# Optimization experiments

Hardware: AMD Instinct MI355X
Metric: run time of the kernel (lower is better)

The kernel has to match this reference:

```python
import jax, jax.numpy as jnp
import numpy as np

N_NODES = 100000
N_EDGES = 1600000
IN_DIM = 128
HIDDEN = 128
OUT_DIM = 10
N_GRAPHS = 512
N_LAYERS = 3


def setup_inputs() -> dict:
    key = jax.random.key(0)
    ks = jax.random.split(key, 12)
    s_in = 1.0 / np.sqrt(IN_DIM)
    s_h = 1.0 / np.sqrt(HIDDEN)
    return {
        "x": jax.random.normal(ks[0], (N_NODES, IN_DIM), jnp.float32),
        "lin1_w": jax.random.normal(ks[1], (IN_DIM, HIDDEN), jnp.float32) * s_in,
        "lin1_b": jnp.zeros((HIDDEN,), jnp.float32),
        "gcn_w": jax.random.normal(ks[2], (N_LAYERS, HIDDEN, HIDDEN), jnp.float32) * s_h,
        "gcn_b": jnp.zeros((N_LAYERS, HIDDEN), jnp.float32),
        "lin_out_w": jax.random.normal(ks[3], (HIDDEN, HIDDEN), jnp.float32) * s_h,
        "lin_out_b": jnp.zeros((HIDDEN,), jnp.float32),
        "cls_w": jax.random.normal(ks[4], (HIDDEN, OUT_DIM), jnp.float32) * s_h,
        "cls_b": jnp.zeros((OUT_DIM,), jnp.float32),
        "edge_index": jax.random.randint(ks[5], (2, N_EDGES), 0, N_NODES, jnp.int64),
        "batch": jnp.sort(jax.random.randint(ks[6], (N_NODES,), 0, N_GRAPHS, jnp.int64)),
    }


def reference(x, lin1_w, lin1_b, gcn_w, gcn_b, lin_out_w, lin_out_b, cls_w, cls_b, edge_index, batch):
    n = x.shape[0]
    # GCNConv normalization with added self-loops (PyG default)
    row, col = edge_index[0], edge_index[1]
    loop = jnp.arange(n)
    row2 = jnp.concatenate([row, loop])  # source (message origin)
    col2 = jnp.concatenate([col, loop])  # target (aggregation index)
    deg = jax.ops.segment_sum(jnp.ones_like(col2, dtype=x.dtype), col2, num_segments=n)
    dinv = jax.lax.rsqrt(jnp.maximum(deg, 1.0))
    norm = (dinv[row2] * dinv[col2])[:, None]  # [E+N, 1]

    counts = jax.ops.segment_sum(jnp.ones((n,), x.dtype), batch, num_segments=N_GRAPHS)
    counts = jnp.maximum(counts, 1.0)[:, None]

    def readout_mean(h):  # global_mean_pool -> [G, H]
        return jax.ops.segment_sum(h, batch, num_segments=N_GRAPHS) / counts

    # lin1 + elu (dropout = identity in eval mode)
    h = jax.nn.elu(x @ lin1_w + lin1_b)
    reps = readout_mean(h)  # readout_layers[0]; l_sum accumulates layer reps
    for i in range(N_LAYERS):
        hw = h @ gcn_w[i]                       # [N, H]
        msg = norm * hw[row2]                   # gather + scale
        agg = jax.ops.segment_sum(msg, col2, num_segments=n)  # scatter-add
        h = jax.nn.elu(agg + gcn_b[i])          # GCNConv bias then NaOp act
        # pooling op is 'none' (remove_pooling=True): graph unchanged
        reps = reps + readout_mean(h)           # readout_layers[i+1], summed by LaOp 'l_sum'
    g = jax.nn.elu(reps @ lin_out_w + lin_out_b)
    logits = g @ cls_w + cls_b
    return jax.nn.log_softmax(logits, axis=-1)
```

## Files before the change

### kernel.cpp

```cpp
#include <hip/hip_runtime.h>
#include <hip/hip_bf16.h>
#include <math.h>

#define NN 100000
#define NE 1600000
#define HID 128
#define NG 512
#define NB 512
#define RB 196

typedef unsigned short ushort_t;
typedef __attribute__((ext_vector_type(8))) short bf16x8;
typedef __attribute__((ext_vector_type(8))) unsigned short ushort8_t;
typedef __attribute__((ext_vector_type(4))) float f32x4;

__device__ __forceinline__ ushort_t f2bf(float v) {
    unsigned u = __float_as_uint(v);
    unsigned r = (u + 0x7FFF + ((u >> 16) & 1)) >> 16;
    return (ushort_t)r;
}
__device__ __forceinline__ float bf2f(ushort_t u) {
    return __uint_as_float((unsigned)u << 16);
}

__global__ __launch_bounds__(256) void hist_and_prepw(const int* __restrict__ ecol, int* __restrict__ ghist, int E,
                                                      const float* __restrict__ lin1_w,
                                                      const float* __restrict__ gcn_w,
                                                      ushort_t* __restrict__ wt_hi,
                                                      ushort_t* __restrict__ wt_lo) {
    if (blockIdx.x < 512) {
        __shared__ int lh[NB];
        for (int i = threadIdx.x; i < NB; i += 256) lh[i] = 0;
        __syncthreads();
        for (int e = blockIdx.x * 256 + threadIdx.x; e < E; e += 512 * 256)
            atomicAdd(&lh[ecol[e] / RB], 1);
        __syncthreads();
        for (int i = threadIdx.x; i < NB; i += 256) {
            int c = lh[i];
            if (c) atomicAdd(&ghist[i], c);
        }
    } else {
        int mb = blockIdx.x - 512;
        int m = mb >> 3;
        int chunk = mb & 7;
        const float* W = (m == 0) ? lin1_w : gcn_w + (size_t)(m - 1) * 16384;
        ushort_t* hi = wt_hi + (size_t)m * 16384;
        ushort_t* lo = wt_lo + (size_t)m * 16384;
        for (int i = chunk * 2048 + threadIdx.x; i < (chunk + 1) * 2048; i += 256) {
            int j = i & 7;
            int lane = (i >> 3) & 63;
            int ks = (i >> 9) & 3;
            int ct = (i >> 11) & 7;
            int n = ct * 16 + (lane & 15);
            int k = ks * 32 + (lane >> 4) * 8 + j;
            float v = W[k * 128 + n];
            ushort_t h = f2bf(v);
            hi[i] = h;
            lo[i] = f2bf(v - bf2f(h));
        }
    }
}

__global__ __launch_bounds__(NB) void bucket_scan(const int* __restrict__ ghist, int* __restrict__ brp,
                                                  int* __restrict__ gcur, int* __restrict__ rp,
                                                  const int* __restrict__ batch, float* __restrict__ invcnt) {
    __shared__ int s[NB];
    int t = threadIdx.x;
    int v = ghist[t];
    s[t] = v;
    __syncthreads();
    for (int off = 1; off < NB; off <<= 1) {
        int x = (t >= off) ? s[t - off] : 0;
        __syncthreads();
        s[t] += x;
        __syncthreads();
    }
    int ex = s[t] - v;
    brp[t] = ex;
    gcur[t] = ex;
    if (t == NB - 1) { brp[NB] = s[t]; rp[NN] = s[t]; }

    int lo = 0, hi = NN;
    while (lo < hi) { int m = (lo + hi) >> 1; if (batch[m] < t) lo = m + 1; else hi = m; }
    int s0 = lo;
    lo = 0; hi = NN;
    while (lo < hi) { int m = (lo + hi) >> 1; if (batch[m] < t + 1) lo = m + 1; else hi = m; }
    int c = lo - s0;
    invcnt[t] = 1.0f / (float)(c > 0 ? c : 1);
}

#define CHUNK 4096
__global__ __launch_bounds__(256) void partition_edges(const int* __restrict__ erow, const int* __restrict__ ecol,
                                                       int* __restrict__ gcur, unsigned int* __restrict__ pairs, int E) {
    __shared__ int cnt[NB];
    __shared__ int base[NB];
    const int t = threadIdx.x;
    const int e0 = blockIdx.x * CHUNK;
    const int e1 = min(e0 + CHUNK, E);
    for (int i = t; i < NB; i += 256) cnt[i] = 0;
    __syncthreads();
    for (int e = e0 + t; e < e1; e += 256) atomicAdd(&cnt[ecol[e] / RB], 1);
    __syncthreads();
    for (int i = t; i < NB; i += 256) {
        int c = cnt[i];
        base[i] = c ? atomicAdd(&gcur[i], c) : 0;
        cnt[i] = 0;
    }
    __syncthreads();
    for (int e = e0 + t; e < e1; e += 256) {
        int d = ecol[e];
        int b = d / RB;
        int off = atomicAdd(&cnt[b], 1);
        pairs[base[b] + off] = ((unsigned)erow[e] << 8) | (unsigned)(d - b * RB);
    }
}

__global__ __launch_bounds__(256) void bucket_fill(const unsigned int* __restrict__ pairs, const int* __restrict__ brp,
                                                   int* __restrict__ rp, float* __restrict__ dinv,
                                                   int* __restrict__ csrc) {
    __shared__ int cnt[RB];
    __shared__ int cur[RB];
    __shared__ int sc[256];
    const int b = blockIdx.x, t = threadIdx.x;
    const int nbase = b * RB;
    const int s = brp[b], e = brp[b + 1];
    for (int i = t; i < RB; i += 256) cnt[i] = 0;
    __syncthreads();
    for (int i = s + t; i < e; i += 256) atomicAdd(&cnt[pairs[i] & 255u], 1);
    __syncthreads();
    int v = (t < RB) ? cnt[t] : 0;
    sc[t] = v;
    __syncthreads();
    for (int off = 1; off < 256; off <<= 1) {
        int x = (t >= off) ? sc[t - off] : 0;
        __syncthreads();
        sc[t] += x;
        __syncthreads();
    }
    if (t < RB) {
        int ex = s + sc[t] - v;
        int node = nbase + t;
        if (node < NN) {
            rp[node] = ex;
            dinv[node] = rsqrtf((float)v + 1.0f);
        }
        cur[t] = ex;
    }
    __syncthreads();
    for (int i = s + t; i < e; i += 256) {
        unsigned int p = pairs[i];
        int slot = atomicAdd(&cur[p & 255u], 1);
        csrc[slot] = (int)(p >> 8);
    }
}

template<bool F32A, int MODE>
__global__ __launch_bounds__(256) void gemm_mfma(const float* __restrict__ A,
                                                 const ushort_t* __restrict__ a_bf,
                                                 const ushort_t* __restrict__ wt_hi,
                                                 const ushort_t* __restrict__ wt_lo,
                                                 const float* __restrict__ bias,
                                                 const float* __restrict__ dinv,
                                                 ushort_t* __restrict__ out0,
                                                 int N) {
    const int lane = threadIdx.x & 63;
    const int wid = threadIdx.x >> 6;
    const int rowBase = blockIdx.x * 128 + wid * 32;
    const int l15 = lane & 15, lg = lane >> 4;

    f32x4 acc[2][8];
#pragma unroll
    for (int rt = 0; rt < 2; ++rt)
#pragma unroll
        for (int ct = 0; ct < 8; ++ct) acc[rt][ct] = (f32x4){0.f, 0.f, 0.f, 0.f};

#pragma unroll
    for (int ks = 0; ks < 4; ++ks) {
        bf16x8 ahi[2], alo[2];
#pragma unroll
        for (int rt = 0; rt < 2; ++rt) {
            int r = rowBase + rt * 16 + l15;
            if (F32A) {
                float av[8];
                if (r < N) {
                    const float* ap = A + (size_t)r * 128 + ks * 32 + lg * 8;
                    float4 a0 = *(const float4*)(ap);
                    float4 a1 = *(const float4*)(ap + 4);
                    av[0] = a0.x; av[1] = a0.y; av[2] = a0.z; av[3] = a0.w;
                    av[4] = a1.x; av[5] = a1.y; av[6] = a1.z; av[7] = a1.w;
                } else {
#pragma unroll
                    for (int j = 0; j < 8; ++j) av[j] = 0.f;
                }
#pragma unroll
                for (int j = 0; j < 8; ++j) {
                    ushort_t h = f2bf(av[j]);
                    ahi[rt][j] = (short)h;
                    alo[rt][j] = (short)f2bf(av[j] - bf2f(h));
                }
            } else {
                if (r < N) {
                    ahi[rt] = *(const bf16x8*)(a_bf + (size_t)r * 128 + ks * 32 + lg * 8);
                } else {
                    bf16x8 z = {0, 0, 0, 0, 0, 0, 0, 0};
                    ahi[rt] = z;
                }
            }
        }
#pragma unroll
        for (int ct = 0; ct < 8; ++ct) {
            size_t boff = (size_t)(((ct * 4 + ks) * 64 + lane) * 8);
            bf16x8 bhi = *(const bf16x8*)(wt_hi + boff);
            bf16x8 blo = *(const bf16x8*)(wt_lo + boff);
            acc[0][ct] = __builtin_amdgcn_mfma_f32_16x16x32_bf16(ahi[0], bhi, acc[0][ct], 0, 0, 0);
            acc[1][ct] = __builtin_amdgcn_mfma_f32_16x16x32_bf16(ahi[1], bhi, acc[1][ct], 0, 0, 0);
            acc[0][ct] = __builtin_amdgcn_mfma_f32_16x16x32_bf16(ahi[0], blo, acc[0][ct], 0, 0, 0);
            acc[1][ct] = __builtin_amdgcn_mfma_f32_16x16x32_bf16(ahi[1], blo, acc[1][ct], 0, 0, 0);
            if (F32A) {
                acc[0][ct] = __builtin_amdgcn_mfma_f32_16x16x32_bf16(alo[0], bhi, acc[0][ct], 0, 0, 0);
                acc[1][ct] = __builtin_amdgcn_mfma_f32_16x16x32_bf16(alo[1], bhi, acc[1][ct], 0, 0, 0);
            }
        }
    }

#pragma unroll
    for (int rt = 0; rt < 2; ++rt) {
#pragma unroll
        for (int reg = 0; reg < 4; ++reg) {
            int row = rowBase + rt * 16 + lg * 4 + reg;
            if (row >= N) continue;
            if (MODE == 0) {
#pragma unroll
                for (int ct = 0; ct < 8; ++ct) {
                    int colc = ct * 16 + l15;
                    float v = acc[rt][ct][reg] + bias[colc];
                    v = v > 0.f ? v : expf(v) - 1.f;
                    out0[(size_t)row * 128 + colc] = f2bf(v);
                }
            } else {
                float dv = dinv[row];
#pragma unroll
                for (int ct = 0; ct < 8; ++ct) {
                    int colc = ct * 16 + l15;
                    out0[(size_t)row * 128 + colc] = f2bf(acc[rt][ct][reg] * dv);
                }
            }
        }
    }
}

__global__ __launch_bounds__(256) void gather_agg(const int* __restrict__ rp,
                                                  const int* __restrict__ csrc,
                                                  const float* __restrict__ dinv,
                                                  const ushort_t* __restrict__ hwb,
                                                  const float* __restrict__ bias,
                                                  const int* __restrict__ batch,
                                                  const float* __restrict__ invcnt,
                                                  float* __restrict__ reps,
                                                  ushort_t* __restrict__ h_out) {
    __shared__ float sh[16][128];
    __shared__ int gid[16];
    const int v0 = blockIdx.x * 16;
    const int ns = (int)(threadIdx.x >> 4);
    int v = v0 + ns;
    int c8 = (int)(threadIdx.x & 15) << 3;
    if (threadIdx.x < 16) {
        int bidx = v0 + (int)threadIdx.x;
        if (bidx > NN - 1) bidx = NN - 1;
        gid[threadIdx.x] = batch[bidx];
    }

    float acc[8] = {};
    if (v < NN) {
        int s = rp[v], e = rp[v + 1];
        int i = s;
        for (; i + 16 <= e; i += 16) {
            int u[16];
#pragma unroll
            for (int k = 0; k < 16; ++k) u[k] = csrc[i + k];
            ushort8_t r[16];
#pragma unroll
            for (int k = 0; k < 16; ++k) r[k] = *(const ushort8_t*)(hwb + (size_t)u[k] * 128 + c8);
#pragma unroll
            for (int k = 0; k < 16; ++k)
#pragma unroll
                for (int j = 0; j < 8; ++j) acc[j] += bf2f(r[k][j]);
        }
        for (; i + 8 <= e; i += 8) {
            int u[8];
#pragma unroll
            for (int k = 0; k < 8; ++k) u[k] = csrc[i + k];
            ushort8_t r[8];
#pragma unroll
            for (int k = 0; k < 8; ++k) r[k] = *(const ushort8_t*)(hwb + (size_t)u[k] * 128 + c8);
#pragma unroll
            for (int k = 0; k < 8; ++k)
#pragma unroll
                for (int j = 0; j < 8; ++j) acc[j] += bf2f(r[k][j]);
        }
        for (; i < e; ++i) {
            int u = csrc[i];
            ushort8_t r0 = *(const ushort8_t*)(hwb + (size_t)u * 128 + c8);
#pragma unroll
            for (int j = 0; j < 8; ++j) acc[j] += bf2f(r0[j]);
        }

        float di = dinv[v];
        ushort8_t sv = *(const ushort8_t*)(hwb + (size_t)v * 128 + c8);
        ushort8_t o;
#pragma unroll
        for (int j = 0; j < 8; ++j) {
            float t = di * (acc[j] + bf2f(sv[j])) + bias[c8 + j];
            t = t > 0.f ? t : expf(t) - 1.f;
            acc[j] = t;
            o[j] = f2bf(t);
        }
        *(ushort8_t*)(h_out + (size_t)v * 128 + c8) = o;
    } else {
#pragma unroll
        for (int j = 0; j < 8; ++j) acc[j] = 0.f;
    }

#pragma unroll
    for (int j = 0; j < 8; ++j) sh[ns][c8 + j] = acc[j];
    __syncthreads();
    if (threadIdx.x < 128) {
        int c = (int)threadIdx.x;
        int nvalid = NN - v0;
        if (nvalid > 16) nvalid = 16;
        float run = sh[0][c];
        int cg = gid[0];
        for (int k = 1; k < nvalid; ++k) {
            int g2 = gid[k];
            if (g2 != cg) {
                unsafeAtomicAdd(&reps[(size_t)cg * 128 + c], run * invcnt[cg]);
                run = 0.f;
                cg = g2;
            }
            run += sh[k][c];
        }
        unsafeAtomicAdd(&reps[(size_t)cg * 128 + c], run * invcnt[cg]);
    }
}

__global__ __launch_bounds__(256) void readout(const ushort_t* __restrict__ h,
                                               const int* __restrict__ batch,
                                               int n, float* __restrict__ reps) {
    int g = blockIdx.x >> 2;
    int part = blockIdx.x & 3;
    int lo = 0, hi = n;
    while (lo < hi) { int m = (lo + hi) >> 1; if (batch[m] < g) lo = m + 1; else hi = m; }
    int s = lo;
    lo = 0; hi = n;
    while (lo < hi) { int m = (lo + hi) >> 1; if (batch[m] < g + 1) lo = m + 1; else hi = m; }
    int e = lo;

    __shared__ float sh[16][128];
    int ns = (int)(threadIdx.x >> 4);
    int L  = (int)(threadIdx.x & 15);
    int c8 = L << 3;
    float acc[8] = {};
    for (int v = s + part + ns * 4; v < e; v += 64) {
        ushort8_t t = *(const ushort8_t*)(h + (size_t)v * 128 + c8);
#pragma unroll
        for (int j = 0; j < 8; ++j) acc[j] += bf2f(t[j]);
    }
#pragma unroll
    for (int j = 0; j < 8; ++j) sh[ns][c8 + j] = acc[j];
    __syncthreads();
    if (threadIdx.x < 128) {
        int c = (int)threadIdx.x;
        float sum = 0.f;
#pragma unroll
        for (int k = 0; k < 16; ++k) sum += sh[k][c];
        float cnt = (float)(e - s > 0 ? e - s : 1);
        unsafeAtomicAdd(&reps[(size_t)g * 128 + c], sum / cnt);
    }
}

__global__ __launch_bounds__(256) void gemm128(const float* __restrict__ A,
                                               const float* __restrict__ W,
                                               const float* __restrict__ bias,
                                               float* __restrict__ out,
                                               int N, int applyElu) {
    __shared__ float xs[64][128];
    __shared__ float ws[128][64];
    const int tid = threadIdx.x;
    const int rowBase = blockIdx.x * 64;
    const int colBase = blockIdx.y * 64;
#pragma unroll
    for (int it = 0; it < 8; ++it) {
        int idx = it * 256 + tid;
        int r = idx >> 5;
        int c4 = (idx & 31) << 2;
        int gr = rowBase + r;
        float4 v = make_float4(0.f, 0.f, 0.f, 0.f);
        if (gr < N) v = *(const float4*)(A + (size_t)gr * 128 + c4);
        *(float4*)(&xs[r][c4]) = v;
    }
#pragma unroll
    for (int it = 0; it < 8; ++it) {
        int idx = it * 256 + tid;
        int k = idx >> 4;
        int c4 = (idx & 15) << 2;
        *(float4*)(&ws[k][c4]) = *(const float4*)(W + (size_t)k * 128 + colBase + c4);
    }
    __syncthreads();
    const int rowg = tid >> 4, colg = tid & 15;
    const int r0 = rowg * 4, c0 = colg * 4;
    float acc[4][4] = {};
#pragma unroll 2
    for (int kb = 0; kb < 128; kb += 4) {
        float4 xr[4], wr[4];
#pragma unroll
        for (int i = 0; i < 4; ++i) xr[i] = *(const float4*)(&xs[r0 + i][kb]);
#pragma unroll
        for (int kk = 0; kk < 4; ++kk) wr[kk] = *(const float4*)(&ws[kb + kk][c0]);
#pragma unroll
        for (int i = 0; i < 4; ++i) {
            const float* xp = (const float*)&xr[i];
#pragma unroll
            for (int kk = 0; kk < 4; ++kk) {
                float xv = xp[kk];
                acc[i][0] = fmaf(xv, wr[kk].x, acc[i][0]);
                acc[i][1] = fmaf(xv, wr[kk].y, acc[i][1]);
                acc[i][2] = fmaf(xv, wr[kk].z, acc[i][2]);
                acc[i][3] = fmaf(xv, wr[kk].w, acc[i][3]);
            }
        }
    }
    float4 b4 = make_float4(0.f, 0.f, 0.f, 0.f);
    if (bias) b4 = *(const float4*)(bias + colBase + c0);
#pragma unroll
    for (int i = 0; i < 4; ++i) {
        int gr = rowBase + r0 + i;
        if (gr < N) {
            float4 o;
            o.x = acc[i][0] + b4.x;
            o.y = acc[i][1] + b4.y;
            o.z = acc[i][2] + b4.z;
            o.w = acc[i][3] + b4.w;
            if (applyElu) {
                o.x = o.x > 0.f ? o.x : expf(o.x) - 1.f;
                o.y = o.y > 0.f ? o.y : expf(o.y) - 1.f;
                o.z = o.z > 0.f ? o.z : expf(o.z) - 1.f;
                o.w = o.w > 0.f ? o.w : expf(o.w) - 1.f;
            }
            *(float4*)(out + (size_t)gr * 128 + colBase + c0) = o;
        }
    }
}

__global__ __launch_bounds__(64) void cls_logsoftmax(const float* __restrict__ g,
                                                     const float* __restrict__ cw,
                                                     const float* __restrict__ cb,
                                                     float* __restrict__ out) {
    int r = blockIdx.x;
    __shared__ float row[128];
    __shared__ float lg[10];
    int t = threadIdx.x;
    row[t] = g[(size_t)r * 128 + t];
    row[64 + t] = g[(size_t)r * 128 + 64 + t];
    __syncthreads();
    if (t < 10) {
        float a = cb[t];
        for (int k = 0; k < 128; ++k) a = fmaf(row[k], cw[k * 10 + t], a);
        lg[t] = a;
    }
    __syncthreads();
    if (t == 0) {
        float m = lg[0];
#pragma unroll
        for (int j = 1; j < 10; ++j) m = fmaxf(m, lg[j]);
        float se = 0.f;
#pragma unroll
        for (int j = 0; j < 10; ++j) se += expf(lg[j] - m);
        float L = logf(se);
#pragma unroll
        for (int j = 0; j < 10; ++j) out[(size_t)r * 10 + j] = lg[j] - m - L;
    }
}

extern "C" void kernel_launch(void* const* d_in, const int* in_sizes, int n_in,
                              void* d_out, int out_size, void* d_ws, size_t ws_size,
                              hipStream_t stream) {
    const float* x        = (const float*)d_in[0];
    const float* lin1_w   = (const float*)d_in[1];
    const float* lin1_b   = (const float*)d_in[2];
    const float* gcn_w    = (const float*)d_in[3];
    const float* gcn_b    = (const float*)d_in[4];
    const float* lin_out_w= (const float*)d_in[5];
    const float* lin_out_b= (const float*)d_in[6];
    const float* cls_w    = (const float*)d_in[7];
    const float* cls_b    = (const float*)d_in[8];
    const int*   ei       = (const int*)d_in[9];
    const int*   batch    = (const int*)d_in[10];
    float* out = (float*)d_out;

    const int* erow = ei;
    const int* ecol = ei + NE;

    ushort_t* h     = (ushort_t*)d_ws;
    ushort_t* hwb   = h + (size_t)NN * 128;
    float*    dinv  = (float*)(hwb + (size_t)NN * 128);
    float*    reps  = dinv + NN;
    float*    gbuf  = reps + (size_t)NG * 128;
    float*    invcnt= gbuf + (size_t)NG * 128;
    int*      rp    = (int*)(invcnt + NG);
    int*      csrc  = rp + NN + 1;
    int*      ghist = csrc + NE;
    int*      brp   = ghist + NB;
    int*      gcur  = brp + NB + 1;
    ushort_t* wt_hi = (ushort_t*)(gcur + NB);
    ushort_t* wt_lo = wt_hi + 4 * 16384;
    unsigned int* pairs = (unsigned int*)(wt_lo + 4 * 16384);

    hipMemsetAsync(ghist, 0, NB * sizeof(int), stream);
    hipMemsetAsync(reps, 0, (size_t)NG * 128 * sizeof(float), stream);

    hist_and_prepw<<<512 + 32, 256, 0, stream>>>(ecol, ghist, NE, lin1_w, gcn_w, wt_hi, wt_lo);
    bucket_scan<<<1, NB, 0, stream>>>(ghist, brp, gcur, rp, batch, invcnt);
    partition_edges<<<(NE + CHUNK - 1) / CHUNK, 256, 0, stream>>>(erow, ecol, gcur, pairs, NE);
    bucket_fill<<<NB, 256, 0, stream>>>(pairs, brp, rp, dinv, csrc);

    const int GEMM_GRID = (NN + 127) / 128;

    gemm_mfma<true, 0><<<GEMM_GRID, 256, 0, stream>>>(x, nullptr, wt_hi, wt_lo,
                                                      lin1_b, dinv, h, NN);
    readout<<<NG * 4, 256, 0, stream>>>(h, batch, NN, reps);

    for (int i = 0; i < 3; ++i) {
        gemm_mfma<false, 1><<<GEMM_GRID, 256, 0, stream>>>(nullptr, h,
                                                           wt_hi + (size_t)(i + 1) * 16384,
                                                           wt_lo + (size_t)(i + 1) * 16384,
                                                           nullptr, dinv, hwb, NN);
        gather_agg<<<(NN + 15) / 16, 256, 0, stream>>>(rp, csrc, dinv, hwb,
                                                       gcn_b + (size_t)i * 128,
                                                       batch, invcnt, reps, h);
    }

    dim3 gs((NG + 63) / 64, 2);
    gemm128<<<gs, 256, 0, stream>>>(reps, lin_out_w, lin_out_b, gbuf, NG, 1);
    cls_logsoftmax<<<NG, 64, 0, stream>>>(gbuf, cls_w, cls_b, out);
}
```

Baseline: 449.9 us.

## Merge independent kernels, tile node-feature layout, and fuse head layers

Runs edge partitioning alongside the first linear GEMM in one launch, and the CSR bucket fill alongside the first readout in another, so independent work shares a grid. The bf16 node-feature buffer is stored in 16-row tiles so GEMM A-loads and gather writes are contiguous per 16-node block. The output linear layer and the classifier with log-softmax become one kernel, and shared-memory rows are padded to avoid bank conflicts. Fewer launches and better overlap come at the cost of heterogeneous blocks in the merged grids and a layout that every consumer must index consistently.

```diff
diff --git a/kernel.cpp b/kernel.cpp
--- a/kernel.cpp
+++ b/kernel.cpp
@@ -8,6 +8,9 @@
 #define NG 512
 #define NB 512
 #define RB 196
+#define CHUNK 4096
+#define NPART ((NE + CHUNK - 1) / CHUNK)
+#define GEMM_GRID ((NN + 127) / 128)
 
 typedef unsigned short ushort_t;
 typedef __attribute__((ext_vector_type(8))) short bf16x8;
@@ -22,6 +25,7 @@
 __device__ __forceinline__ float bf2f(ushort_t u) {
     return __uint_as_float((unsigned)u << 16);
 }
+
 
 __global__ __launch_bounds__(256) void hist_and_prepw(const int* __restrict__ ecol, int* __restrict__ ghist, int E,
                                                       const float* __restrict__ lin1_w,
@@ -89,83 +93,20 @@
     invcnt[t] = 1.0f / (float)(c > 0 ? c : 1);
 }
 
-#define CHUNK 4096
-__global__ __launch_bounds__(256) void partition_edges(const int* __restrict__ erow, const int* __restrict__ ecol,
-                                                       int* __restrict__ gcur, unsigned int* __restrict__ pairs, int E) {
-    __shared__ int cnt[NB];
-    __shared__ int base[NB];
-    const int t = threadIdx.x;
-    const int e0 = blockIdx.x * CHUNK;
-    const int e1 = min(e0 + CHUNK, E);
-    for (int i = t; i < NB; i += 256) cnt[i] = 0;
-    __syncthreads();
-    for (int e = e0 + t; e < e1; e += 256) atomicAdd(&cnt[ecol[e] / RB], 1);
-    __syncthreads();
-    for (int i = t; i < NB; i += 256) {
-        int c = cnt[i];
-        base[i] = c ? atomicAdd(&gcur[i], c) : 0;
-        cnt[i] = 0;
-    }
-    __syncthreads();
-    for (int e = e0 + t; e < e1; e += 256) {
-        int d = ecol[e];
-        int b = d / RB;
-        int off = atomicAdd(&cnt[b], 1);
-        pairs[base[b] + off] = ((unsigned)erow[e] << 8) | (unsigned)(d - b * RB);
-    }
-}
-
-__global__ __launch_bounds__(256) void bucket_fill(const unsigned int* __restrict__ pairs, const int* __restrict__ brp,
-                                                   int* __restrict__ rp, float* __restrict__ dinv,
-                                                   int* __restrict__ csrc) {
-    __shared__ int cnt[RB];
-    __shared__ int cur[RB];
-    __shared__ int sc[256];
-    const int b = blockIdx.x, t = threadIdx.x;
-    const int nbase = b * RB;
-    const int s = brp[b], e = brp[b + 1];
-    for (int i = t; i < RB; i += 256) cnt[i] = 0;
-    __syncthreads();
-    for (int i = s + t; i < e; i += 256) atomicAdd(&cnt[pairs[i] & 255u], 1);
-    __syncthreads();
-    int v = (t < RB) ? cnt[t] : 0;
-    sc[t] = v;
-    __syncthreads();
-    for (int off = 1; off < 256; off <<= 1) {
-        int x = (t >= off) ? sc[t - off] : 0;
-        __syncthreads();
-        sc[t] += x;
-        __syncthreads();
-    }
-    if (t < RB) {
-        int ex = s + sc[t] - v;
-        int node = nbase + t;
-        if (node < NN) {
-            rp[node] = ex;
-            dinv[node] = rsqrtf((float)v + 1.0f);
-        }
-        cur[t] = ex;
-    }
-    __syncthreads();
-    for (int i = s + t; i < e; i += 256) {
-        unsigned int p = pairs[i];
-        int slot = atomicAdd(&cur[p & 255u], 1);
-        csrc[slot] = (int)(p >> 8);
-    }
-}
-
 template<bool F32A, int MODE>
-__global__ __launch_bounds__(256) void gemm_mfma(const float* __restrict__ A,
-                                                 const ushort_t* __restrict__ a_bf,
-                                                 const ushort_t* __restrict__ wt_hi,
-                                                 const ushort_t* __restrict__ wt_lo,
-                                                 const float* __restrict__ bias,
-                                                 const float* __restrict__ dinv,
-                                                 ushort_t* __restrict__ out0,
-                                                 int N) {
-    const int lane = threadIdx.x & 63;
-    const int wid = threadIdx.x >> 6;
-    const int rowBase = blockIdx.x * 128 + wid * 32;
+__device__ __forceinline__ void gemm_body(int bid, int tid,
+                                          const float* __restrict__ A,
+                                          const ushort_t* __restrict__ a_bf,
+                                          const ushort_t* __restrict__ wt_hi,
+                                          const ushort_t* __restrict__ wt_lo,
+                                          const float* __restrict__ bias,
+                                          const float* __restrict__ dinv,
+                                          ushort_t* __restrict__ out0,
+                                          int N) {
+    const int lane = tid & 63;
+    const int wid = tid >> 6;
+    const int rowBase = bid * 128 + wid * 32;
+    const int rblk = rowBase >> 4;
     const int l15 = lane & 15, lg = lane >> 4;
 
     f32x4 acc[2][8];
@@ -200,7 +141,7 @@
                 }
             } else {
                 if (r < N) {
-                    ahi[rt] = *(const bf16x8*)(a_bf + (size_t)r * 128 + ks * 32 + lg * 8);
+                    ahi[rt] = *(const bf16x8*)(a_bf + (size_t)(rblk + rt) * 2048 + (ks * 4 + lg) * 128 + l15 * 8);
                 } else {
                     bf16x8 z = {0, 0, 0, 0, 0, 0, 0, 0};
                     ahi[rt] = z;
@@ -230,12 +171,13 @@
             int row = rowBase + rt * 16 + lg * 4 + reg;
             if (row >= N) continue;
             if (MODE == 0) {
+                int r16 = lg * 4 + reg;
 #pragma unroll
                 for (int ct = 0; ct < 8; ++ct) {
                     int colc = ct * 16 + l15;
                     float v = acc[rt][ct][reg] + bias[colc];
                     v = v > 0.f ? v : expf(v) - 1.f;
-                    out0[(size_t)row * 128 + colc] = f2bf(v);
+                    out0[(size_t)(rblk + rt) * 2048 + (colc >> 3) * 128 + r16 * 8 + (colc & 7)] = f2bf(v);
                 }
             } else {
                 float dv = dinv[row];
@@ -247,6 +189,126 @@
             }
         }
     }
+}
+
+__global__ __launch_bounds__(256) void part_gemm1(const int* __restrict__ erow, const int* __restrict__ ecol,
+                                                  int* __restrict__ gcur, unsigned int* __restrict__ pairs, int E,
+                                                  const float* __restrict__ x,
+                                                  const ushort_t* __restrict__ wt_hi,
+                                                  const ushort_t* __restrict__ wt_lo,
+                                                  const float* __restrict__ lin1_b,
+                                                  ushort_t* __restrict__ h) {
+    if (blockIdx.x < NPART) {
+        __shared__ int cnt[NB];
+        __shared__ int base[NB];
+        const int t = threadIdx.x;
+        const int e0 = blockIdx.x * CHUNK;
+        const int e1 = min(e0 + CHUNK, E);
+        for (int i = t; i < NB; i += 256) cnt[i] = 0;
+        __syncthreads();
+        for (int e = e0 + t; e < e1; e += 256) atomicAdd(&cnt[ecol[e] / RB], 1);
+        __syncthreads();
+        for (int i = t; i < NB; i += 256) {
+            int c = cnt[i];
+            base[i] = c ? atomicAdd(&gcur[i], c) : 0;
+            cnt[i] = 0;
+        }
+        __syncthreads();
+        for (int e = e0 + t; e < e1; e += 256) {
+            int d = ecol[e];
+            int b = d / RB;
+            int off = atomicAdd(&cnt[b], 1);
+            pairs[base[b] + off] = ((unsigned)erow[e] << 8) | (unsigned)(d - b * RB);
+        }
+    } else {
+        gemm_body<true, 0>(blockIdx.x - NPART, threadIdx.x, x, nullptr, wt_hi, wt_lo,
+                           lin1_b, nullptr, h, NN);
+    }
+}
+
+__global__ __launch_bounds__(256) void fill_readout0(const unsigned int* __restrict__ pairs, const int* __restrict__ brp,
+                                                     int* __restrict__ rp, float* __restrict__ dinv,
+                                                     int* __restrict__ csrc,
+                                                     const ushort_t* __restrict__ h,
+                                                     const int* __restrict__ batch,
+                                                     const float* __restrict__ invcnt,
+                                                     float* __restrict__ reps) {
+    if (blockIdx.x < NB) {
+        __shared__ int cnt[RB];
+        __shared__ int cur[RB];
+        __shared__ int sc[256];
+        const int b = blockIdx.x, t = threadIdx.x;
+        const int nbase = b * RB;
+        const int s = brp[b], e = brp[b + 1];
+        for (int i = t; i < RB; i += 256) cnt[i] = 0;
+        __syncthreads();
+        for (int i = s + t; i < e; i += 256) atomicAdd(&cnt[pairs[i] & 255u], 1);
+        __syncthreads();
+        int v = (t < RB) ? cnt[t] : 0;
+        sc[t] = v;
+        __syncthreads();
+        for (int off = 1; off < 256; off <<= 1) {
+            int x = (t >= off) ? sc[t - off] : 0;
+            __syncthreads();
+            sc[t] += x;
+            __syncthreads();
+        }
+        if (t < RB) {
+            int ex = s + sc[t] - v;
+            int node = nbase + t;
+            if (node < NN) {
+                rp[node] = ex;
+                dinv[node] = rsqrtf((float)v + 1.0f);
+            }
+            cur[t] = ex;
+        }
+        __syncthreads();
+        for (int i = s + t; i < e; i += 256) {
+            unsigned int p = pairs[i];
+            int slot = atomicAdd(&cur[p & 255u], 1);
+            csrc[slot] = (int)(p >> 8);
+        }
+    } else {
+        int bb = blockIdx.x - NB;
+        int g = bb >> 2;
+        int part = bb & 3;
+        int lo = 0, hi = NN;
+        while (lo < hi) { int m = (lo + hi) >> 1; if (batch[m] < g) lo = m + 1; else hi = m; }
+        int s = lo;
+        lo = 0; hi = NN;
+        while (lo < hi) { int m = (lo + hi) >> 1; if (batch[m] < g + 1) lo = m + 1; else hi = m; }
+        int e = lo;
+
+        __shared__ float sh[16][136];
+        int ns = (int)(threadIdx.x >> 4);
+        int L  = (int)(threadIdx.x & 15);
+        int c8 = L << 3;
+        float acc[8] = {};
+        for (int v = s + part + ns * 4; v < e; v += 64) {
+            ushort8_t t = *(const ushort8_t*)(h + (size_t)(v >> 4) * 2048 + L * 128 + (v & 15) * 8);
+#pragma unroll
+            for (int j = 0; j < 8; ++j) acc[j] += bf2f(t[j]);
+        }
+#pragma unroll
+        for (int j = 0; j < 8; ++j) sh[ns][c8 + j] = acc[j];
+        __syncthreads();
+        if (threadIdx.x < 128) {
+            int c = (int)threadIdx.x;
+            float sum = 0.f;
+#pragma unroll
+            for (int k = 0; k < 16; ++k) sum += sh[k][c];
+            unsafeAtomicAdd(&reps[(size_t)g * 128 + c], sum * invcnt[g]);
+        }
+    }
+}
+
+__global__ __launch_bounds__(256) void gemm_gcn(const ushort_t* __restrict__ a_bf,
+                                                const ushort_t* __restrict__ wt_hi,
+                                                const ushort_t* __restrict__ wt_lo,
+                                                const float* __restrict__ dinv,
+                                                ushort_t* __restrict__ hwb) {
+    gemm_body<false, 1>(blockIdx.x, threadIdx.x, nullptr, a_bf, wt_hi, wt_lo,
+                        nullptr, dinv, hwb, NN);
 }
 
 __global__ __launch_bounds__(256) void gather_agg(const int* __restrict__ rp,
@@ -258,12 +320,13 @@
                                                   const float* __restrict__ invcnt,
                                                   float* __restrict__ reps,
                                                   ushort_t* __restrict__ h_out) {
-    __shared__ float sh[16][128];
+    __shared__ float sh[16][136];
     __shared__ int gid[16];
     const int v0 = blockIdx.x * 16;
     const int ns = (int)(threadIdx.x >> 4);
     int v = v0 + ns;
-    int c8 = (int)(threadIdx.x & 15) << 3;
+    int L = (int)(threadIdx.x & 15);
+    int c8 = L << 3;
     if (threadIdx.x < 16) {
         int bidx = v0 + (int)threadIdx.x;
         if (bidx > NN - 1) bidx = NN - 1;
@@ -315,7 +378,7 @@
             acc[j] = t;
             o[j] = f2bf(t);
         }
-        *(ushort8_t*)(h_out + (size_t)v * 128 + c8) = o;
+        *(ushort8_t*)(h_out + (size_t)blockIdx.x * 2048 + L * 128 + ns * 8) = o;
     } else {
 #pragma unroll
         for (int j = 0; j < 8; ++j) acc[j] = 0.f;
@@ -343,129 +406,28 @@
     }
 }
 
-__global__ __launch_bounds__(256) void readout(const ushort_t* __restrict__ h,
-                                               const int* __restrict__ batch,
-                                               int n, float* __restrict__ reps) {
-    int g = blockIdx.x >> 2;
-    int part = blockIdx.x & 3;
-    int lo = 0, hi = n;
-    while (lo < hi) { int m = (lo + hi) >> 1; if (batch[m] < g) lo = m + 1; else hi = m; }
-    int s = lo;
-    lo = 0; hi = n;
-    while (lo < hi) { int m = (lo + hi) >> 1; if (batch[m] < g + 1) lo = m + 1; else hi = m; }
-    int e = lo;
-
-    __shared__ float sh[16][128];
-    int ns = (int)(threadIdx.x >> 4);
-    int L  = (int)(threadIdx.x & 15);
-    int c8 = L << 3;
-    float acc[8] = {};
-    for (int v = s + part + ns * 4; v < e; v += 64) {
-        ushort8_t t = *(const ushort8_t*)(h + (size_t)v * 128 + c8);
-#pragma unroll
-        for (int j = 0; j < 8; ++j) acc[j] += bf2f(t[j]);
-    }
-#pragma unroll
-    for (int j = 0; j < 8; ++j) sh[ns][c8 + j] = acc[j];
-    __syncthreads();
-    if (threadIdx.x < 128) {
-        int c = (int)threadIdx.x;
-        float sum = 0.f;
-#pragma unroll
-        for (int k = 0; k < 16; ++k) sum += sh[k][c];
-        float cnt = (float)(e - s > 0 ? e - s : 1);
-        unsafeAtomicAdd(&reps[(size_t)g * 128 + c], sum / cnt);
-    }
-}
-
-__global__ __launch_bounds__(256) void gemm128(const float* __restrict__ A,
-                                               const float* __restrict__ W,
-                                               const float* __restrict__ bias,
-                                               float* __restrict__ out,
-                                               int N, int applyElu) {
-    __shared__ float xs[64][128];
-    __shared__ float ws[128][64];
-    const int tid = threadIdx.x;
-    const int rowBase = blockIdx.x * 64;
-    const int colBase = blockIdx.y * 64;
-#pragma unroll
-    for (int it = 0; it < 8; ++it) {
-        int idx = it * 256 + tid;
-        int r = idx >> 5;
-        int c4 = (idx & 31) << 2;
-        int gr = rowBase + r;
-        float4 v = make_float4(0.f, 0.f, 0.f, 0.f);
-        if (gr < N) v = *(const float4*)(A + (size_t)gr * 128 + c4);
-        *(float4*)(&xs[r][c4]) = v;
-    }
-#pragma unroll
-    for (int it = 0; it < 8; ++it) {
-        int idx = it * 256 + tid;
-        int k = idx >> 4;
-        int c4 = (idx & 15) << 2;
-        *(float4*)(&ws[k][c4]) = *(const float4*)(W + (size_t)k * 128 + colBase + c4);
-    }
-    __syncthreads();
-    const int rowg = tid >> 4, colg = tid & 15;
-    const int r0 = rowg * 4, c0 = colg * 4;
-    float acc[4][4] = {};
-#pragma unroll 2
-    for (int kb = 0; kb < 128; kb += 4) {
-        float4 xr[4], wr[4];
-#pragma unroll
-        for (int i = 0; i < 4; ++i) xr[i] = *(const float4*)(&xs[r0 + i][kb]);
-#pragma unroll
-        for (int kk = 0; kk < 4; ++kk) wr[kk] = *(const float4*)(&ws[kb + kk][c0]);
-#pragma unroll
-        for (int i = 0; i < 4; ++i) {
-            const float* xp = (const float*)&xr[i];
-#pragma unroll
-            for (int kk = 0; kk < 4; ++kk) {
-                float xv = xp[kk];
-                acc[i][0] = fmaf(xv, wr[kk].x, acc[i][0]);
-                acc[i][1] = fmaf(xv, wr[kk].y, acc[i][1]);
-                acc[i][2] = fmaf(xv, wr[kk].z, acc[i][2]);
-                acc[i][3] = fmaf(xv, wr[kk].w, acc[i][3]);
-            }
-        }
-    }
-    float4 b4 = make_float4(0.f, 0.f, 0.f, 0.f);
-    if (bias) b4 = *(const float4*)(bias + colBase + c0);
-#pragma unroll
-    for (int i = 0; i < 4; ++i) {
-        int gr = rowBase + r0 + i;
-        if (gr < N) {
-            float4 o;
-            o.x = acc[i][0] + b4.x;
-            o.y = acc[i][1] + b4.y;
-            o.z = acc[i][2] + b4.z;
-            o.w = acc[i][3] + b4.w;
-            if (applyElu) {
-                o.x = o.x > 0.f ? o.x : expf(o.x) - 1.f;
-                o.y = o.y > 0.f ? o.y : expf(o.y) - 1.f;
-                o.z = o.z > 0.f ? o.z : expf(o.z) - 1.f;
-                o.w = o.w > 0.f ? o.w : expf(o.w) - 1.f;
-            }
-            *(float4*)(out + (size_t)gr * 128 + colBase + c0) = o;
-        }
-    }
-}
-
-__global__ __launch_bounds__(64) void cls_logsoftmax(const float* __restrict__ g,
-                                                     const float* __restrict__ cw,
-                                                     const float* __restrict__ cb,
-                                                     float* __restrict__ out) {
-    int r = blockIdx.x;
-    __shared__ float row[128];
+__global__ __launch_bounds__(128) void head_fused(const float* __restrict__ reps,
+                                                  const float* __restrict__ wout,
+                                                  const float* __restrict__ bout,
+                                                  const float* __restrict__ cw,
+                                                  const float* __restrict__ cb,
+                                                  float* __restrict__ out) {
+    __shared__ float rrow[128];
+    __shared__ float gg[128];
     __shared__ float lg[10];
     int t = threadIdx.x;
-    row[t] = g[(size_t)r * 128 + t];
-    row[64 + t] = g[(size_t)r * 128 + 64 + t];
+    int g = blockIdx.x;
+    rrow[t] = reps[(size_t)g * 128 + t];
+    __syncthreads();
+    float a = bout[t];
+    for (int k = 0; k < 128; ++k) a = fmaf(rrow[k], wout[k * 128 + t], a);
+    a = a > 0.f ? a : expf(a) - 1.f;
+    gg[t] = a;
     __syncthreads();
     if (t < 10) {
-        float a = cb[t];
-        for (int k = 0; k < 128; ++k) a = fmaf(row[k], cw[k * 10 + t], a);
-        lg[t] = a;
+        float s = cb[t];
+        for (int k = 0; k < 128; ++k) s = fmaf(gg[k], cw[k * 10 + t], s);
+        lg[t] = s;
     }
     __syncthreads();
     if (t == 0) {
@@ -477,7 +439,7 @@
         for (int j = 0; j < 10; ++j) se += expf(lg[j] - m);
         float L = logf(se);
 #pragma unroll
-        for (int j = 0; j < 10; ++j) out[(size_t)r * 10 + j] = lg[j] - m - L;
+        for (int j = 0; j < 10; ++j) out[(size_t)g * 10 + j] = lg[j] - m - L;
     }
 }
 
@@ -504,8 +466,7 @@
     ushort_t* hwb   = h + (size_t)NN * 128;
     float*    dinv  = (float*)(hwb + (size_t)NN * 128);
     float*    reps  = dinv + NN;
-    float*    gbuf  = reps + (size_t)NG * 128;
-    float*    invcnt= gbuf + (size_t)NG * 128;
+    float*    invcnt= reps + (size_t)NG * 128;
     int*      rp    = (int*)(invcnt + NG);
     int*      csrc  = rp + NN + 1;
     int*      ghist = csrc + NE;
@@ -520,26 +481,19 @@
 
     hist_and_prepw<<<512 + 32, 256, 0, stream>>>(ecol, ghist, NE, lin1_w, gcn_w, wt_hi, wt_lo);
     bucket_scan<<<1, NB, 0, stream>>>(ghist, brp, gcur, rp, batch, invcnt);
-    partition_edges<<<(NE + CHUNK - 1) / CHUNK, 256, 0, stream>>>(erow, ecol, gcur, pairs, NE);
-    bucket_fill<<<NB, 256, 0, stream>>>(pairs, brp, rp, dinv, csrc);
-
-    const int GEMM_GRID = (NN + 127) / 128;
-
-    gemm_mfma<true, 0><<<GEMM_GRID, 256, 0, stream>>>(x, nullptr, wt_hi, wt_lo,
-                                                      lin1_b, dinv, h, NN);
-    readout<<<NG * 4, 256, 0, stream>>>(h, batch, NN, reps);
+    part_gemm1<<<NPART + GEMM_GRID, 256, 0, stream>>>(erow, ecol, gcur, pairs, NE,
+                                                      x, wt_hi, wt_lo, lin1_b, h);
+    fill_readout0<<<NB + NG * 4, 256, 0, stream>>>(pairs, brp, rp, dinv, csrc,
+                                                   h, batch, invcnt, reps);
 
     for (int i = 0; i < 3; ++i) {
-        gemm_mfma<false, 1><<<GEMM_GRID, 256, 0, stream>>>(nullptr, h,
-                                                           wt_hi + (size_t)(i + 1) * 16384,
-                                                           wt_lo + (size_t)(i + 1) * 16384,
-                                                           nullptr, dinv, hwb, NN);
+        gemm_gcn<<<GEMM_GRID, 256, 0, stream>>>(h, wt_hi + (size_t)(i + 1) * 16384,
+                                                wt_lo + (size_t)(i + 1) * 16384,
+                                                dinv, hwb);
         gather_agg<<<(NN + 15) / 16, 256, 0, stream>>>(rp, csrc, dinv, hwb,
                                                        gcn_b + (size_t)i * 128,
                                                        batch, invcnt, reps, h);
     }
 
-    dim3 gs((NG + 63) / 64, 2);
-    gemm128<<<gs, 256, 0, stream>>>(reps, lin_out_w, lin_out_b, gbuf, NG, 1);
-    cls_logsoftmax<<<NG, 64, 0, stream>>>(gbuf, cls_w, cls_b, out);
-}
+    head_fused<<<NG, 128, 0, stream>>>(reps, lin_out_w, lin_out_b, cls_w, cls_b, out);
+}
```

Result: faster. 434.2 us (-3.5%).
